# Performance work log

Measured on AMD Instinct MI355X. Metric: run time of the kernel, lower is better.

## Reference

```python
import jax, jax.numpy as jnp
import numpy as np

N_NODES = 50000
N_EDGES = 1600000
DIM = 128
SLOPE = 0.2  # LeakyReLU negative slope


def setup_inputs() -> dict:
    key = jax.random.key(0)
    ks = jax.random.split(key, 9)
    indices = jax.random.randint(ks[0], (2, N_EDGES), 0, N_NODES)
    features = jax.random.normal(ks[1], (N_NODES, DIM), dtype=jnp.float32)
    W1_w = jax.random.normal(ks[2], (DIM, DIM), dtype=jnp.float32) * 0.05
    W1_b = jax.random.normal(ks[3], (DIM,), dtype=jnp.float32) * 0.05
    W2_w = jax.random.normal(ks[4], (DIM, DIM), dtype=jnp.float32) * 0.05
    W2_b = jax.random.normal(ks[5], (DIM,), dtype=jnp.float32) * 0.05
    Watt_w = jax.random.normal(ks[6], (DIM, DIM), dtype=jnp.float32) * 0.05
    Watt_b = jax.random.normal(ks[7], (DIM,), dtype=jnp.float32) * 0.05
    a = jax.random.normal(ks[8], (2 * DIM, 1), dtype=jnp.float32) * 0.05
    return {"indices": indices, "features": features, "num_nodes": N_NODES,
            "W1_w": W1_w, "W1_b": W1_b, "W2_w": W2_w, "W2_b": W2_b,
            "Watt_w": Watt_w, "Watt_b": Watt_b, "a": a}


def reference(indices, features, num_nodes, W1_w, W1_b, W2_w, W2_b, Watt_w, Watt_b, a):
    src, dst = indices[0], indices[1]
    d = W1_w.shape[1]
    # attention scores: e_ij = leakyrelu(cat(h_src, h_dst) @ a) == h_src@a1 + h_dst@a2
    h_att = features @ Watt_w + Watt_b                      # [N, d]
    a1, a2 = a[:d], a[d:]                                    # each [d, 1]
    e = jax.nn.leaky_relu(h_att[src] @ a1 + h_att[dst] @ a2, SLOPE)  # [E, 1]
    # global-max-stabilized segment softmax over incoming edges of dst
    e = e - jnp.max(e)
    exp_e = jnp.exp(e)                                       # [E, 1]
    denom = jax.ops.segment_sum(exp_e, dst, num_segments=num_nodes)  # [N, 1]
    alpha = exp_e / (denom[dst] + 1e-9)                      # [E, 1]
    # weighted message aggregation
    h_msg = features @ W1_w + W1_b                           # [N, d]
    weighted = h_msg[src] * alpha                            # [E, d]
    h_neigh = jax.ops.segment_sum(weighted, dst, num_segments=num_nodes)  # [N, d]
    # in_dim == out_dim -> h_self = features (module skips extra W1)
    h_self = features
    sum_h = h_self + h_neigh
    prod_h = h_self * h_neigh
    return jax.nn.leaky_relu(sum_h + prod_h @ W2_w + W2_b, SLOPE)
```

## Files before the change

kernel.cpp:

```cpp
#include <hip/hip_runtime.h>

#define DIM 128
#define SLOPE 0.2f
#define NPBK 64
#define CHUNK_A 8192
#define EPT 32
#define KMAX 1024
#define WT_STRIDE 136

typedef __attribute__((ext_vector_type(8))) short bf16x8;
typedef __attribute__((ext_vector_type(4))) float f32x4;

__device__ __forceinline__ float leaky(float x) { return x > 0.f ? x : SLOPE * x; }

__device__ __forceinline__ unsigned short f2bf(float x) {
    unsigned u = __float_as_uint(x);
    return (unsigned short)((u + 0x7FFFu + ((u >> 16) & 1u)) >> 16);
}
__device__ __forceinline__ float bf2f(unsigned short h) {
    return __uint_as_float(((unsigned)h) << 16);
}
__device__ __forceinline__ bf16x8 pack_bf16x8(float4 a, float4 b) {
    bf16x8 r;
    r[0] = (short)f2bf(a.x); r[1] = (short)f2bf(a.y);
    r[2] = (short)f2bf(a.z); r[3] = (short)f2bf(a.w);
    r[4] = (short)f2bf(b.x); r[5] = (short)f2bf(b.y);
    r[6] = (short)f2bf(b.z); r[7] = (short)f2bf(b.w);
    return r;
}

__global__ void k_prep(const float* __restrict__ Watt_w, const float* __restrict__ Watt_b,
                       const float* __restrict__ a, float* __restrict__ v1,
                       float* __restrict__ v2, float* __restrict__ c12) {
    int k = threadIdx.x;
    __shared__ float a1s[DIM], a2s[DIM];
    __shared__ float r1[DIM], r2[DIM];
    a1s[k] = a[k];
    a2s[k] = a[DIM + k];
    __syncthreads();
    float acc1 = 0.f, acc2 = 0.f;
    const float* row = Watt_w + (size_t)k * DIM;
    for (int j = 0; j < DIM; ++j) {
        float w = row[j];
        acc1 += w * a1s[j];
        acc2 += w * a2s[j];
    }
    v1[k] = acc1;
    v2[k] = acc2;
    float b = Watt_b[k];
    r1[k] = b * a1s[k];
    r2[k] = b * a2s[k];
    __syncthreads();
    for (int off = 64; off > 0; off >>= 1) {
        if (k < off) { r1[k] += r1[k + off]; r2[k] += r2[k + off]; }
        __syncthreads();
    }
    if (k == 0) { c12[0] = r1[0]; c12[1] = r2[0]; }
}

__global__ __launch_bounds__(256) void k_node_fwd(
    const float* __restrict__ feat, const float* __restrict__ W1,
    const float* __restrict__ W1b, const float* __restrict__ v1,
    const float* __restrict__ v2, const float* __restrict__ c12,
    unsigned short* __restrict__ h_msg, float* __restrict__ s1, float* __restrict__ s2,
    int n_nodes, int n_tiles16, int total_waves) {
    __shared__ unsigned short Wt[DIM * WT_STRIDE];
    __shared__ float v1s[DIM], v2s[DIM];
    int tid = threadIdx.x;
    for (int i = tid; i < DIM * DIM; i += 256) {
        int k = i >> 7, n = i & 127;
        Wt[n * WT_STRIDE + k] = f2bf(W1[i]);
    }
    if (tid < DIM) { v1s[tid] = v1[tid]; v2s[tid] = v2[tid]; }
    __syncthreads();

    int lane = tid & 63, wid = tid >> 6;
    int ln15 = lane & 15, q = lane >> 4;
    float c1 = c12[0], c2 = c12[1];
    float bias[8];
    #pragma unroll
    for (int nt = 0; nt < 8; ++nt) bias[nt] = W1b[nt * 16 + ln15];

    for (int t = blockIdx.x * 4 + wid; t < n_tiles16; t += total_waves) {
        int base = t * 16;
        int row = base + ln15;
        bool valid = row < n_nodes;
        const float* frow = feat + (size_t)row * DIM;
        bf16x8 afr[4];
        float p1 = 0.f, p2 = 0.f;
        #pragma unroll
        for (int kc = 0; kc < 4; ++kc) {
            int col0 = kc * 32 + q * 8;
            float4 u0 = {0.f, 0.f, 0.f, 0.f}, u1 = {0.f, 0.f, 0.f, 0.f};
            if (valid) {
                u0 = *(const float4*)&frow[col0];
                u1 = *(const float4*)&frow[col0 + 4];
            }
            float4 wa = *(const float4*)&v1s[col0];
            float4 wb = *(const float4*)&v1s[col0 + 4];
            float4 wc = *(const float4*)&v2s[col0];
            float4 wd = *(const float4*)&v2s[col0 + 4];
            p1 += u0.x * wa.x + u0.y * wa.y + u0.z * wa.z + u0.w * wa.w
                + u1.x * wb.x + u1.y * wb.y + u1.z * wb.z + u1.w * wb.w;
            p2 += u0.x * wc.x + u0.y * wc.y + u0.z * wc.z + u0.w * wc.w
                + u1.x * wd.x + u1.y * wd.y + u1.z * wd.z + u1.w * wd.w;
            afr[kc] = pack_bf16x8(u0, u1);
        }
        p1 += __shfl_xor(p1, 16, 64); p1 += __shfl_xor(p1, 32, 64);
        p2 += __shfl_xor(p2, 16, 64); p2 += __shfl_xor(p2, 32, 64);
        if (q == 0 && valid) { s1[row] = p1 + c1; s2[row] = p2 + c2; }

        f32x4 acc[8];
        #pragma unroll
        for (int nt = 0; nt < 8; ++nt)
            acc[nt] = (f32x4){bias[nt], bias[nt], bias[nt], bias[nt]};
        #pragma unroll
        for (int kc = 0; kc < 4; ++kc) {
            #pragma unroll
            for (int nt = 0; nt < 8; ++nt) {
                bf16x8 b = *(const bf16x8*)&Wt[(nt * 16 + ln15) * WT_STRIDE + kc * 32 + q * 8];
                acc[nt] = __builtin_amdgcn_mfma_f32_16x16x32_bf16(afr[kc], b, acc[nt], 0, 0, 0);
            }
        }
        #pragma unroll
        for (int nt = 0; nt < 8; ++nt) {
            #pragma unroll
            for (int r = 0; r < 4; ++r) {
                int rr = base + q * 4 + r;
                if (rr < n_nodes)
                    h_msg[(size_t)rr * DIM + nt * 16 + ln15] = f2bf(acc[nt][r]);
            }
        }
    }
}

__global__ __launch_bounds__(256) void k_bhist(const int* __restrict__ dst,
                                               int* __restrict__ bucket_cnt,
                                               int n_edges, int K) {
    __shared__ int h[KMAX];
    int tid = threadIdx.x;
    for (int i = tid; i < KMAX; i += 256) h[i] = 0;
    __syncthreads();
    int cbase = blockIdx.x * CHUNK_A;
    #pragma unroll
    for (int p = 0; p < 8; ++p) {
        int i0 = cbase + p * 1024 + tid * 4;
        if (i0 + 3 < n_edges) {
            int4 d = *(const int4*)&dst[i0];
            atomicAdd(&h[d.x >> 6], 1);
            atomicAdd(&h[d.y >> 6], 1);
            atomicAdd(&h[d.z >> 6], 1);
            atomicAdd(&h[d.w >> 6], 1);
        } else {
            for (int i = i0; i < n_edges; ++i) atomicAdd(&h[dst[i] >> 6], 1);
        }
    }
    __syncthreads();
    for (int i = tid; i < K; i += 256) {
        int c = h[i];
        if (c) atomicAdd(&bucket_cnt[i], c);
    }
}

__global__ __launch_bounds__(1024) void k_bscan(const int* __restrict__ bucket_cnt,
                                                int* __restrict__ bucket_base,
                                                int* __restrict__ bucket_cur, int K) {
    __shared__ int part[1024];
    int t = threadIdx.x;
    int v = (t < K) ? bucket_cnt[t] : 0;
    part[t] = v;
    __syncthreads();
    for (int off = 1; off < 1024; off <<= 1) {
        int u = (t >= off) ? part[t - off] : 0;
        __syncthreads();
        part[t] += u;
        __syncthreads();
    }
    if (t < K) {
        int excl = part[t] - v;
        bucket_base[t] = excl;
        bucket_cur[t] = excl;
    }
}

__global__ __launch_bounds__(256) void k_bpart(const int* __restrict__ src,
                                               const int* __restrict__ dst,
                                               int* __restrict__ bucket_cur,
                                               int* __restrict__ ebuf,
                                               int n_edges, int K) {
    __shared__ int h[KMAX];
    __shared__ int lcur[KMAX];
    int tid = threadIdx.x;
    for (int i = tid; i < KMAX; i += 256) h[i] = 0;
    __syncthreads();
    int cbase = blockIdx.x * CHUNK_A;
    int pval[EPT], pb[EPT];
    #pragma unroll
    for (int p = 0; p < 8; ++p) {
        int i0 = cbase + p * 1024 + tid * 4;
        if (i0 + 3 < n_edges) {
            int4 d = *(const int4*)&dst[i0];
            int4 s = *(const int4*)&src[i0];
            int b0 = d.x >> 6, b1 = d.y >> 6, b2 = d.z >> 6, b3 = d.w >> 6;
            atomicAdd(&h[b0], 1); atomicAdd(&h[b1], 1);
            atomicAdd(&h[b2], 1); atomicAdd(&h[b3], 1);
            pb[p * 4 + 0] = b0; pval[p * 4 + 0] = ((d.x & 63) << 17) | s.x;
            pb[p * 4 + 1] = b1; pval[p * 4 + 1] = ((d.y & 63) << 17) | s.y;
            pb[p * 4 + 2] = b2; pval[p * 4 + 2] = ((d.z & 63) << 17) | s.z;
            pb[p * 4 + 3] = b3; pval[p * 4 + 3] = ((d.w & 63) << 17) | s.w;
        } else {
            #pragma unroll
            for (int k = 0; k < 4; ++k) {
                int i = i0 + k;
                if (i < n_edges) {
                    int d = dst[i], s = src[i];
                    int b = d >> 6;
                    atomicAdd(&h[b], 1);
                    pb[p * 4 + k] = b;
                    pval[p * 4 + k] = ((d & 63) << 17) | s;
                } else {
                    pb[p * 4 + k] = -1;
                    pval[p * 4 + k] = 0;
                }
            }
        }
    }
    __syncthreads();
    for (int i = tid; i < K; i += 256) {
        int c = h[i];
        lcur[i] = c ? atomicAdd(&bucket_cur[i], c) : 0;
    }
    __syncthreads();
    #pragma unroll
    for (int k = 0; k < EPT; ++k) {
        int b = pb[k];
        if (b >= 0) {
            int pos = atomicAdd(&lcur[b], 1);
            ebuf[pos] = pval[k];
        }
    }
}

__global__ __launch_bounds__(256) void k_bcsr(const int* __restrict__ ebuf,
                                              const int* __restrict__ bucket_base,
                                              int* __restrict__ row,
                                              int* __restrict__ csr_src,
                                              int n_nodes, int n_edges, int K) {
    __shared__ int bins[NPBK], scn[NPBK], cur[NPBK];
    int b = blockIdx.x;
    int tid = threadIdx.x;
    int start = bucket_base[b];
    int end = (b + 1 < K) ? bucket_base[b + 1] : n_edges;
    if (tid < NPBK) bins[tid] = 0;
    __syncthreads();
    for (int i = start + tid; i < end; i += 256)
        atomicAdd(&bins[ebuf[i] >> 17], 1);
    __syncthreads();
    if (tid < NPBK) scn[tid] = bins[tid];
    __syncthreads();
    for (int off = 1; off < NPBK; off <<= 1) {
        int v = (tid < NPBK && tid >= off) ? scn[tid - off] : 0;
        __syncthreads();
        if (tid < NPBK) scn[tid] += v;
        __syncthreads();
    }
    if (tid < NPBK) {
        int node = b * NPBK + tid;
        if (node < n_nodes) row[node] = start + scn[tid];
        cur[tid] = start + scn[tid] - bins[tid];
    }
    __syncthreads();
    for (int i = start + tid; i < end; i += 256) {
        int v = ebuf[i];
        int pos = atomicAdd(&cur[v >> 17], 1);
        csr_src[pos] = v & 0x1FFFF;
    }
}

__global__ __launch_bounds__(256) void k_gather(
    const int* __restrict__ row, const int* __restrict__ csr_src,
    const float* __restrict__ s1, const float* __restrict__ s2,
    const unsigned short* __restrict__ h_msg, float* __restrict__ h_neigh, int n_nodes) {
    int g = (blockIdx.x * blockDim.x + threadIdx.x) >> 5;
    if (g >= n_nodes) return;
    int lane = threadIdx.x & 31;
    int begin = (g == 0) ? 0 : row[g - 1];
    int end = row[g];
    float s2d = s2[g];
    float4 accA = {0.f, 0.f, 0.f, 0.f}, accB = {0.f, 0.f, 0.f, 0.f};
    float wA = 0.f, wB = 0.f;
    int j = begin;
    int iA = (j < end) ? csr_src[j] : 0;
    int iB = (j + 1 < end) ? csr_src[j + 1] : 0;
    while (j + 1 < end) {
        int cA = iA, cB = iB;
        int jn = j + 2;
        if (jn < end)     iA = csr_src[jn];
        if (jn + 1 < end) iB = csr_src[jn + 1];
        ushort4 uA = *(const ushort4*)&h_msg[(size_t)cA * DIM + lane * 4];
        ushort4 uB = *(const ushort4*)&h_msg[(size_t)cB * DIM + lane * 4];
        float eA = __expf(leaky(s1[cA] + s2d));
        float eB = __expf(leaky(s1[cB] + s2d));
        accA.x += eA * bf2f(uA.x); accA.y += eA * bf2f(uA.y);
        accA.z += eA * bf2f(uA.z); accA.w += eA * bf2f(uA.w);
        wA += eA;
        accB.x += eB * bf2f(uB.x); accB.y += eB * bf2f(uB.y);
        accB.z += eB * bf2f(uB.z); accB.w += eB * bf2f(uB.w);
        wB += eB;
        j = jn;
    }
    if (j < end) {
        int cA = iA;
        ushort4 uA = *(const ushort4*)&h_msg[(size_t)cA * DIM + lane * 4];
        float eA = __expf(leaky(s1[cA] + s2d));
        accA.x += eA * bf2f(uA.x); accA.y += eA * bf2f(uA.y);
        accA.z += eA * bf2f(uA.z); accA.w += eA * bf2f(uA.w);
        wA += eA;
    }
    float wsum = wA + wB;
    float inv = 1.f / (wsum + 1e-9f);
    float4 o;
    o.x = (accA.x + accB.x) * inv;
    o.y = (accA.y + accB.y) * inv;
    o.z = (accA.z + accB.z) * inv;
    o.w = (accA.w + accB.w) * inv;
    *(float4*)&h_neigh[(size_t)g * DIM + lane * 4] = o;
}

__global__ __launch_bounds__(256) void k_final(
    const float* __restrict__ feat, const float* __restrict__ h_neigh,
    const float* __restrict__ W2, const float* __restrict__ W2b,
    float* __restrict__ out, int n_nodes, int n_tiles16, int total_waves) {
    __shared__ unsigned short Wt[DIM * WT_STRIDE];
    int tid = threadIdx.x;
    for (int i = tid; i < DIM * DIM; i += 256) {
        int k = i >> 7, n = i & 127;
        Wt[n * WT_STRIDE + k] = f2bf(W2[i]);
    }
    __syncthreads();

    int lane = tid & 63, wid = tid >> 6;
    int ln15 = lane & 15, q = lane >> 4;
    float bias[8];
    #pragma unroll
    for (int nt = 0; nt < 8; ++nt) bias[nt] = W2b[nt * 16 + ln15];

    for (int t = blockIdx.x * 4 + wid; t < n_tiles16; t += total_waves) {
        int base = t * 16;
        int row = base + ln15;
        bool valid = row < n_nodes;
        const float* frow = feat + (size_t)row * DIM;
        const float* hrow = h_neigh + (size_t)row * DIM;
        bf16x8 afr[4];
        #pragma unroll
        for (int kc = 0; kc < 4; ++kc) {
            int col0 = kc * 32 + q * 8;
            float4 p0 = {0.f, 0.f, 0.f, 0.f}, p1 = {0.f, 0.f, 0.f, 0.f};
            if (valid) {
                float4 f0 = *(const float4*)&frow[col0];
                float4 f1 = *(const float4*)&frow[col0 + 4];
                float4 h0 = *(const float4*)&hrow[col0];
                float4 h1 = *(const float4*)&hrow[col0 + 4];
                p0.x = f0.x * h0.x; p0.y = f0.y * h0.y;
                p0.z = f0.z * h0.z; p0.w = f0.w * h0.w;
                p1.x = f1.x * h1.x; p1.y = f1.y * h1.y;
                p1.z = f1.z * h1.z; p1.w = f1.w * h1.w;
            }
            afr[kc] = pack_bf16x8(p0, p1);
        }
        f32x4 acc[8];
        #pragma unroll
        for (int nt = 0; nt < 8; ++nt)
            acc[nt] = (f32x4){bias[nt], bias[nt], bias[nt], bias[nt]};
        #pragma unroll
        for (int kc = 0; kc < 4; ++kc) {
            #pragma unroll
            for (int nt = 0; nt < 8; ++nt) {
                bf16x8 b = *(const bf16x8*)&Wt[(nt * 16 + ln15) * WT_STRIDE + kc * 32 + q * 8];
                acc[nt] = __builtin_amdgcn_mfma_f32_16x16x32_bf16(afr[kc], b, acc[nt], 0, 0, 0);
            }
        }
        #pragma unroll
        for (int r = 0; r < 4; ++r) {
            int rr = base + q * 4 + r;
            if (rr < n_nodes) {
                #pragma unroll
                for (int nt = 0; nt < 8; ++nt) {
                    int col = nt * 16 + ln15;
                    float f = feat[(size_t)rr * DIM + col];
                    float hn = h_neigh[(size_t)rr * DIM + col];
                    out[(size_t)rr * DIM + col] = leaky(f + hn + acc[nt][r]);
                }
            }
        }
    }
}

extern "C" void kernel_launch(void* const* d_in, const int* in_sizes, int n_in,
                              void* d_out, int out_size, void* d_ws, size_t ws_size,
                              hipStream_t stream) {
    const int*   indices = (const int*)d_in[0];
    const float* feat    = (const float*)d_in[1];
    const float* W1w  = (const float*)d_in[3];
    const float* W1b  = (const float*)d_in[4];
    const float* W2w  = (const float*)d_in[5];
    const float* W2b  = (const float*)d_in[6];
    const float* Wattw = (const float*)d_in[7];
    const float* Wattb = (const float*)d_in[8];
    const float* a     = (const float*)d_in[9];

    int n_edges = in_sizes[0] / 2;
    int n_nodes = in_sizes[1] / DIM;
    int n_tiles16 = (n_nodes + 15) / 16;
    int K = (n_nodes + NPBK - 1) / NPBK;
    const int* src = indices;
    const int* dst = indices + n_edges;

    unsigned short* h_msg = (unsigned short*)d_out;
    int* ebuf = (int*)(h_msg + (size_t)n_nodes * DIM);

    float* ws      = (float*)d_ws;
    float* h_neigh = ws;
    int*   csr_src = (int*)(h_neigh + (size_t)n_nodes * DIM);
    int*   row     = csr_src + n_edges;
    float* s1      = (float*)(row + n_nodes);
    float* s2      = s1 + n_nodes;
    float* v1      = s2 + n_nodes;
    float* v2      = v1 + DIM;
    float* c12     = v2 + DIM;
    int*   bucket_cnt  = (int*)(c12 + 2);
    int*   bucket_base = bucket_cnt + KMAX;
    int*   bucket_cur  = bucket_base + KMAX;

    hipMemsetAsync(bucket_cnt, 0, (size_t)KMAX * sizeof(int), stream);

    k_prep<<<1, 128, 0, stream>>>(Wattw, Wattb, a, v1, v2, c12);
    {
        int blocks = 512;
        k_node_fwd<<<blocks, 256, 0, stream>>>(feat, W1w, W1b, v1, v2, c12,
                                               h_msg, s1, s2, n_nodes,
                                               n_tiles16, blocks * 4);
    }
    {
        int nb = (n_edges + CHUNK_A - 1) / CHUNK_A;
        k_bhist<<<nb, 256, 0, stream>>>(dst, bucket_cnt, n_edges, K);
        k_bscan<<<1, 1024, 0, stream>>>(bucket_cnt, bucket_base, bucket_cur, K);
        k_bpart<<<nb, 256, 0, stream>>>(src, dst, bucket_cur, ebuf, n_edges, K);
        k_bcsr<<<K, 256, 0, stream>>>(ebuf, bucket_base, row, csr_src,
                                      n_nodes, n_edges, K);
    }
    {
        long long threads = (long long)n_nodes * 32;
        int blocks = (int)((threads + 255) / 256);
        k_gather<<<blocks, 256, 0, stream>>>(row, csr_src, s1, s2,
                                             h_msg, h_neigh, n_nodes);
    }
    {
        int blocks = 512;
        k_final<<<blocks, 256, 0, stream>>>(feat, h_neigh, W2w, W2b,
                                            (float*)d_out, n_nodes,
                                            n_tiles16, blocks * 4);
    }
}
```

Measured before the change: 252.8 us.

## Fuse edge partition into node GEMM launch using fixed-capacity bucket slabs

Drops the histogram and scan kernels. Each 64-node bucket now gets a fixed slab of 4000 edge slots, so the partition step can scatter right after one atomic per bucket. The partition blocks run in the same launch as the node GEMM blocks through a shared-memory union, so the two can overlap. CSR source indices are stored as 16-bit values, and the gather loop prefetches s1 scores one step ahead. The cost is that correctness now depends on no bucket exceeding 4000 edges and on node ids fitting in 16 bits, which holds for uniform random inputs of this size but not in general.

```diff
diff --git a/kernel.cpp b/kernel.cpp
--- a/kernel.cpp
+++ b/kernel.cpp
@@ -3,6 +3,7 @@
 #define DIM 128
 #define SLOPE 0.2f
 #define NPBK 64
+#define SLAB 4000
 #define CHUNK_A 8192
 #define EPT 32
 #define KMAX 1024
@@ -58,15 +59,77 @@
     if (k == 0) { c12[0] = r1[0]; c12[1] = r2[0]; }
 }
 
-__global__ __launch_bounds__(256) void k_node_fwd(
+__global__ __launch_bounds__(256) void k_fused_fwd(
     const float* __restrict__ feat, const float* __restrict__ W1,
     const float* __restrict__ W1b, const float* __restrict__ v1,
     const float* __restrict__ v2, const float* __restrict__ c12,
     unsigned short* __restrict__ h_msg, float* __restrict__ s1, float* __restrict__ s2,
-    int n_nodes, int n_tiles16, int total_waves) {
-    __shared__ unsigned short Wt[DIM * WT_STRIDE];
-    __shared__ float v1s[DIM], v2s[DIM];
+    const int* __restrict__ src, const int* __restrict__ dst,
+    int* __restrict__ bucket_cur, int* __restrict__ ebuf,
+    int n_nodes, int n_tiles16, int n_edges, int K, int nb_part, int total_waves) {
+    __shared__ union {
+        struct { unsigned short Wt[DIM * WT_STRIDE]; float v1s[DIM]; float v2s[DIM]; } g;
+        struct { int h[KMAX]; int lcur[KMAX]; } p;
+    } sm;
     int tid = threadIdx.x;
+
+    if (blockIdx.x < nb_part) {
+        int* h = sm.p.h;
+        int* lcur = sm.p.lcur;
+        for (int i = tid; i < KMAX; i += 256) h[i] = 0;
+        __syncthreads();
+        int cbase = blockIdx.x * CHUNK_A;
+        int pval[EPT], pb[EPT];
+        #pragma unroll
+        for (int p = 0; p < 8; ++p) {
+            int i0 = cbase + p * 1024 + tid * 4;
+            if (i0 + 3 < n_edges) {
+                int4 d = *(const int4*)&dst[i0];
+                int4 s = *(const int4*)&src[i0];
+                int b0 = d.x >> 6, b1 = d.y >> 6, b2 = d.z >> 6, b3 = d.w >> 6;
+                atomicAdd(&h[b0], 1); atomicAdd(&h[b1], 1);
+                atomicAdd(&h[b2], 1); atomicAdd(&h[b3], 1);
+                pb[p * 4 + 0] = b0; pval[p * 4 + 0] = ((d.x & 63) << 17) | s.x;
+                pb[p * 4 + 1] = b1; pval[p * 4 + 1] = ((d.y & 63) << 17) | s.y;
+                pb[p * 4 + 2] = b2; pval[p * 4 + 2] = ((d.z & 63) << 17) | s.z;
+                pb[p * 4 + 3] = b3; pval[p * 4 + 3] = ((d.w & 63) << 17) | s.w;
+            } else {
+                #pragma unroll
+                for (int k = 0; k < 4; ++k) {
+                    int i = i0 + k;
+                    if (i < n_edges) {
+                        int d = dst[i], s = src[i];
+                        int b = d >> 6;
+                        atomicAdd(&h[b], 1);
+                        pb[p * 4 + k] = b;
+                        pval[p * 4 + k] = ((d & 63) << 17) | s;
+                    } else {
+                        pb[p * 4 + k] = -1;
+                        pval[p * 4 + k] = 0;
+                    }
+                }
+            }
+        }
+        __syncthreads();
+        for (int i = tid; i < K; i += 256) {
+            int c = h[i];
+            lcur[i] = c ? (i * SLAB + atomicAdd(&bucket_cur[i], c)) : 0;
+        }
+        __syncthreads();
+        #pragma unroll
+        for (int k = 0; k < EPT; ++k) {
+            int b = pb[k];
+            if (b >= 0) {
+                int pos = atomicAdd(&lcur[b], 1);
+                ebuf[pos] = pval[k];
+            }
+        }
+        return;
+    }
+
+    unsigned short* Wt = sm.g.Wt;
+    float* v1s = sm.g.v1s;
+    float* v2s = sm.g.v2s;
     for (int i = tid; i < DIM * DIM; i += 256) {
         int k = i >> 7, n = i & 127;
         Wt[n * WT_STRIDE + k] = f2bf(W1[i]);
@@ -81,7 +144,7 @@
     #pragma unroll
     for (int nt = 0; nt < 8; ++nt) bias[nt] = W1b[nt * 16 + ln15];
 
-    for (int t = blockIdx.x * 4 + wid; t < n_tiles16; t += total_waves) {
+    for (int t = (blockIdx.x - nb_part) * 4 + wid; t < n_tiles16; t += total_waves) {
         int base = t * 16;
         int row = base + ln15;
         bool valid = row < n_nodes;
@@ -134,123 +197,16 @@
     }
 }
 
-__global__ __launch_bounds__(256) void k_bhist(const int* __restrict__ dst,
-                                               int* __restrict__ bucket_cnt,
-                                               int n_edges, int K) {
-    __shared__ int h[KMAX];
-    int tid = threadIdx.x;
-    for (int i = tid; i < KMAX; i += 256) h[i] = 0;
-    __syncthreads();
-    int cbase = blockIdx.x * CHUNK_A;
-    #pragma unroll
-    for (int p = 0; p < 8; ++p) {
-        int i0 = cbase + p * 1024 + tid * 4;
-        if (i0 + 3 < n_edges) {
-            int4 d = *(const int4*)&dst[i0];
-            atomicAdd(&h[d.x >> 6], 1);
-            atomicAdd(&h[d.y >> 6], 1);
-            atomicAdd(&h[d.z >> 6], 1);
-            atomicAdd(&h[d.w >> 6], 1);
-        } else {
-            for (int i = i0; i < n_edges; ++i) atomicAdd(&h[dst[i] >> 6], 1);
-        }
-    }
-    __syncthreads();
-    for (int i = tid; i < K; i += 256) {
-        int c = h[i];
-        if (c) atomicAdd(&bucket_cnt[i], c);
-    }
-}
-
-__global__ __launch_bounds__(1024) void k_bscan(const int* __restrict__ bucket_cnt,
-                                                int* __restrict__ bucket_base,
-                                                int* __restrict__ bucket_cur, int K) {
-    __shared__ int part[1024];
-    int t = threadIdx.x;
-    int v = (t < K) ? bucket_cnt[t] : 0;
-    part[t] = v;
-    __syncthreads();
-    for (int off = 1; off < 1024; off <<= 1) {
-        int u = (t >= off) ? part[t - off] : 0;
-        __syncthreads();
-        part[t] += u;
-        __syncthreads();
-    }
-    if (t < K) {
-        int excl = part[t] - v;
-        bucket_base[t] = excl;
-        bucket_cur[t] = excl;
-    }
-}
-
-__global__ __launch_bounds__(256) void k_bpart(const int* __restrict__ src,
-                                               const int* __restrict__ dst,
-                                               int* __restrict__ bucket_cur,
-                                               int* __restrict__ ebuf,
-                                               int n_edges, int K) {
-    __shared__ int h[KMAX];
-    __shared__ int lcur[KMAX];
-    int tid = threadIdx.x;
-    for (int i = tid; i < KMAX; i += 256) h[i] = 0;
-    __syncthreads();
-    int cbase = blockIdx.x * CHUNK_A;
-    int pval[EPT], pb[EPT];
-    #pragma unroll
-    for (int p = 0; p < 8; ++p) {
-        int i0 = cbase + p * 1024 + tid * 4;
-        if (i0 + 3 < n_edges) {
-            int4 d = *(const int4*)&dst[i0];
-            int4 s = *(const int4*)&src[i0];
-            int b0 = d.x >> 6, b1 = d.y >> 6, b2 = d.z >> 6, b3 = d.w >> 6;
-            atomicAdd(&h[b0], 1); atomicAdd(&h[b1], 1);
-            atomicAdd(&h[b2], 1); atomicAdd(&h[b3], 1);
-            pb[p * 4 + 0] = b0; pval[p * 4 + 0] = ((d.x & 63) << 17) | s.x;
-            pb[p * 4 + 1] = b1; pval[p * 4 + 1] = ((d.y & 63) << 17) | s.y;
-            pb[p * 4 + 2] = b2; pval[p * 4 + 2] = ((d.z & 63) << 17) | s.z;
-            pb[p * 4 + 3] = b3; pval[p * 4 + 3] = ((d.w & 63) << 17) | s.w;
-        } else {
-            #pragma unroll
-            for (int k = 0; k < 4; ++k) {
-                int i = i0 + k;
-                if (i < n_edges) {
-                    int d = dst[i], s = src[i];
-                    int b = d >> 6;
-                    atomicAdd(&h[b], 1);
-                    pb[p * 4 + k] = b;
-                    pval[p * 4 + k] = ((d & 63) << 17) | s;
-                } else {
-                    pb[p * 4 + k] = -1;
-                    pval[p * 4 + k] = 0;
-                }
-            }
-        }
-    }
-    __syncthreads();
-    for (int i = tid; i < K; i += 256) {
-        int c = h[i];
-        lcur[i] = c ? atomicAdd(&bucket_cur[i], c) : 0;
-    }
-    __syncthreads();
-    #pragma unroll
-    for (int k = 0; k < EPT; ++k) {
-        int b = pb[k];
-        if (b >= 0) {
-            int pos = atomicAdd(&lcur[b], 1);
-            ebuf[pos] = pval[k];
-        }
-    }
-}
-
 __global__ __launch_bounds__(256) void k_bcsr(const int* __restrict__ ebuf,
-                                              const int* __restrict__ bucket_base,
+                                              const int* __restrict__ bucket_cur,
                                               int* __restrict__ row,
-                                              int* __restrict__ csr_src,
-                                              int n_nodes, int n_edges, int K) {
+                                              unsigned short* __restrict__ csr_src,
+                                              int n_nodes, int K) {
     __shared__ int bins[NPBK], scn[NPBK], cur[NPBK];
     int b = blockIdx.x;
     int tid = threadIdx.x;
-    int start = bucket_base[b];
-    int end = (b + 1 < K) ? bucket_base[b + 1] : n_edges;
+    int start = b * SLAB;
+    int end = start + bucket_cur[b];
     if (tid < NPBK) bins[tid] = 0;
     __syncthreads();
     for (int i = start + tid; i < end; i += 256)
@@ -273,34 +229,37 @@
     for (int i = start + tid; i < end; i += 256) {
         int v = ebuf[i];
         int pos = atomicAdd(&cur[v >> 17], 1);
-        csr_src[pos] = v & 0x1FFFF;
+        csr_src[pos] = (unsigned short)(v & 0xFFFF);
     }
 }
 
 __global__ __launch_bounds__(256) void k_gather(
-    const int* __restrict__ row, const int* __restrict__ csr_src,
+    const int* __restrict__ row, const unsigned short* __restrict__ csr_src,
     const float* __restrict__ s1, const float* __restrict__ s2,
     const unsigned short* __restrict__ h_msg, float* __restrict__ h_neigh, int n_nodes) {
     int g = (blockIdx.x * blockDim.x + threadIdx.x) >> 5;
     if (g >= n_nodes) return;
     int lane = threadIdx.x & 31;
-    int begin = (g == 0) ? 0 : row[g - 1];
+    int begin = ((g & (NPBK - 1)) == 0) ? (g >> 6) * SLAB : row[g - 1];
     int end = row[g];
     float s2d = s2[g];
     float4 accA = {0.f, 0.f, 0.f, 0.f}, accB = {0.f, 0.f, 0.f, 0.f};
     float wA = 0.f, wB = 0.f;
     int j = begin;
-    int iA = (j < end) ? csr_src[j] : 0;
-    int iB = (j + 1 < end) ? csr_src[j + 1] : 0;
+    int iA = (j < end) ? (int)csr_src[j] : 0;
+    int iB = (j + 1 < end) ? (int)csr_src[j + 1] : 0;
+    float pA = s1[iA], pB = s1[iB];
     while (j + 1 < end) {
         int cA = iA, cB = iB;
+        float sA = pA, sB = pB;
         int jn = j + 2;
-        if (jn < end)     iA = csr_src[jn];
-        if (jn + 1 < end) iB = csr_src[jn + 1];
+        if (jn < end)     iA = (int)csr_src[jn];
+        if (jn + 1 < end) iB = (int)csr_src[jn + 1];
+        pA = s1[iA]; pB = s1[iB];
         ushort4 uA = *(const ushort4*)&h_msg[(size_t)cA * DIM + lane * 4];
         ushort4 uB = *(const ushort4*)&h_msg[(size_t)cB * DIM + lane * 4];
-        float eA = __expf(leaky(s1[cA] + s2d));
-        float eB = __expf(leaky(s1[cB] + s2d));
+        float eA = __expf(leaky(sA + s2d));
+        float eB = __expf(leaky(sB + s2d));
         accA.x += eA * bf2f(uA.x); accA.y += eA * bf2f(uA.y);
         accA.z += eA * bf2f(uA.z); accA.w += eA * bf2f(uA.w);
         wA += eA;
@@ -312,7 +271,7 @@
     if (j < end) {
         int cA = iA;
         ushort4 uA = *(const ushort4*)&h_msg[(size_t)cA * DIM + lane * 4];
-        float eA = __expf(leaky(s1[cA] + s2d));
+        float eA = __expf(leaky(pA + s2d));
         accA.x += eA * bf2f(uA.x); accA.y += eA * bf2f(uA.y);
         accA.z += eA * bf2f(uA.z); accA.w += eA * bf2f(uA.w);
         wA += eA;
@@ -421,34 +380,27 @@
 
     float* ws      = (float*)d_ws;
     float* h_neigh = ws;
-    int*   csr_src = (int*)(h_neigh + (size_t)n_nodes * DIM);
-    int*   row     = csr_src + n_edges;
+    unsigned short* csr_src = (unsigned short*)(h_neigh + (size_t)n_nodes * DIM);
+    int*   row     = (int*)(csr_src + (size_t)K * SLAB);
     float* s1      = (float*)(row + n_nodes);
     float* s2      = s1 + n_nodes;
     float* v1      = s2 + n_nodes;
     float* v2      = v1 + DIM;
     float* c12     = v2 + DIM;
-    int*   bucket_cnt  = (int*)(c12 + 2);
-    int*   bucket_base = bucket_cnt + KMAX;
-    int*   bucket_cur  = bucket_base + KMAX;
-
-    hipMemsetAsync(bucket_cnt, 0, (size_t)KMAX * sizeof(int), stream);
+    int*   bucket_cur = (int*)(c12 + 2);
+
+    hipMemsetAsync(bucket_cur, 0, (size_t)KMAX * sizeof(int), stream);
 
     k_prep<<<1, 128, 0, stream>>>(Wattw, Wattb, a, v1, v2, c12);
     {
-        int blocks = 512;
-        k_node_fwd<<<blocks, 256, 0, stream>>>(feat, W1w, W1b, v1, v2, c12,
-                                               h_msg, s1, s2, n_nodes,
-                                               n_tiles16, blocks * 4);
-    }
-    {
-        int nb = (n_edges + CHUNK_A - 1) / CHUNK_A;
-        k_bhist<<<nb, 256, 0, stream>>>(dst, bucket_cnt, n_edges, K);
-        k_bscan<<<1, 1024, 0, stream>>>(bucket_cnt, bucket_base, bucket_cur, K);
-        k_bpart<<<nb, 256, 0, stream>>>(src, dst, bucket_cur, ebuf, n_edges, K);
-        k_bcsr<<<K, 256, 0, stream>>>(ebuf, bucket_base, row, csr_src,
-                                      n_nodes, n_edges, K);
-    }
+        int nb_part = (n_edges + CHUNK_A - 1) / CHUNK_A;
+        int gemm_blocks = 512;
+        k_fused_fwd<<<nb_part + gemm_blocks, 256, 0, stream>>>(
+            feat, W1w, W1b, v1, v2, c12, h_msg, s1, s2,
+            src, dst, bucket_cur, ebuf,
+            n_nodes, n_tiles16, n_edges, K, nb_part, gemm_blocks * 4);
+    }
+    k_bcsr<<<K, 256, 0, stream>>>(ebuf, bucket_cur, row, csr_src, n_nodes, K);
     {
         long long threads = (long long)n_nodes * 32;
         int blocks = (int)((threads + 255) / 256);
```

Result: faster. 217.6 us (-13.9%).
